# Performance work log

Hardware: AMD Instinct MI355X
Metric: run time of the kernel (lower is better)

The kernel has to match this reference:

```python
import jax, jax.numpy as jnp
import numpy as np

B, T, D, H = 2, 2048, 1024, 16
DK = D // H  # 64, head dim (even, required by RoPE pairing)


def setup_inputs() -> dict:
    key = jax.random.key(0)
    ks = jax.random.split(key, 9)
    sc = 1.0 / np.sqrt(D)
    x = jax.random.normal(ks[0], (B, T, D), jnp.float32)
    wq = jax.random.normal(ks[1], (D, D), jnp.float32) * sc
    bq = jax.random.normal(ks[2], (D,), jnp.float32) * 0.01
    wk = jax.random.normal(ks[3], (D, D), jnp.float32) * sc
    bk = jax.random.normal(ks[4], (D,), jnp.float32) * 0.01
    wv = jax.random.normal(ks[5], (D, D), jnp.float32) * sc
    bv = jax.random.normal(ks[6], (D,), jnp.float32) * 0.01
    wo = jax.random.normal(ks[7], (D, D), jnp.float32) * sc
    bo = jax.random.normal(ks[8], (D,), jnp.float32) * 0.01
    # causal mask, True = masked (matches masked_fill semantics); dim==3 -> broadcast over heads
    attn_mask = jnp.triu(jnp.ones((T, T), dtype=bool), 1)[None]  # [1,T,T]
    return dict(x=x, wq=wq, bq=bq, wk=wk, bk=bk, wv=wv, bv=bv, wo=wo, bo=bo,
                attn_mask=attn_mask)


def _rope(xh, sin, cos):
    # xh: [B,H,T,DK]; sin/cos: [T,DK/2]
    x1 = xh[..., 0::2]
    x2 = xh[..., 1::2]
    return jnp.stack([x1 * cos - x2 * sin, x1 * sin + x2 * cos], axis=-1).reshape(xh.shape)


def reference(x, wq, bq, wk, bk, wv, bv, wo, bo, attn_mask):
    q = (x @ wq.T + bq).reshape(B, T, H, DK).transpose(0, 2, 1, 3)  # [B,H,T,DK]
    k = (x @ wk.T + bk).reshape(B, T, H, DK).transpose(0, 2, 1, 3)
    v = (x @ wv.T + bv).reshape(B, T, H, DK).transpose(0, 2, 1, 3)
    # RoPE (seq_offset = 0)
    theta = 10000.0 ** (jnp.arange(0, DK, 2, dtype=jnp.float32) / DK)  # [DK/2]
    pos = jnp.arange(T, dtype=jnp.float32)[:, None]                    # [T,1]
    ang = pos / theta                                                  # [T,DK/2]
    sin, cos = jnp.sin(ang), jnp.cos(ang)
    q = _rope(q, sin, cos)
    k = _rope(k, sin, cos)
    # fp32 stable attention (inputs already fp32)
    scores = jnp.einsum('bhtd,bhsd->bhts', q, k) / np.sqrt(DK)
    scores = jnp.where(attn_mask[:, None], -1e9, scores)  # mask broadcast over heads
    attn = jax.nn.softmax(scores, axis=-1)
    ctx = jnp.einsum('bhts,bhsd->bhtd', attn, v)
    ctx = ctx.transpose(0, 2, 1, 3).reshape(B, T, D)
    return ctx @ wo.T + bo
```

## Files before the change

kernel.cpp:

```cpp
#include <hip/hip_runtime.h>
#include <stdint.h>
#include <stddef.h>

#define T_ 2048
#define D_ 1024
#define H_ 16

typedef __attribute__((ext_vector_type(8))) short short8;
typedef __attribute__((ext_vector_type(4))) float f32x4;
typedef __attribute__((ext_vector_type(4))) short s16x4;

__device__ __forceinline__ unsigned short f2bf(float f){
  union { float f; unsigned u; } c; c.f = f;
  unsigned u = c.u;
  return (unsigned short)((u + 0x7fffu + ((u >> 16) & 1u)) >> 16);
}

__device__ __forceinline__ unsigned pk_bf16(float lo, float hi){
  unsigned r;
  asm("v_cvt_pk_bf16_f32 %0, %1, %2" : "=v"(r) : "v"(lo), "v"(hi));
  return r;
}

__device__ __forceinline__ float fexp2(float x){
#if __has_builtin(__builtin_amdgcn_exp2f)
  return __builtin_amdgcn_exp2f(x);
#else
  return exp2f(x);
#endif
}

__device__ __forceinline__ f32x4 mfma16(short8 a, short8 b, f32x4 c){
  return __builtin_amdgcn_mfma_f32_16x16x32_bf16(a, b, c, 0, 0, 0);
}

__device__ __forceinline__ void gload16(const void* g, void* l){
  __builtin_amdgcn_global_load_lds(
      (const __attribute__((address_space(1))) unsigned*)g,
      (__attribute__((address_space(3))) unsigned*)l, 16, 0, 0);
}

__global__ __launch_bounds__(256) void k_prep(const float* __restrict__ x,
    const float* __restrict__ wq, const float* __restrict__ wk,
    const float* __restrict__ wv, const float* __restrict__ wo,
    unsigned short* __restrict__ xb, unsigned short* __restrict__ wqkv,
    unsigned short* __restrict__ wob, float* __restrict__ tab)
{
  if (blockIdx.x < 256){
    int i = blockIdx.x * 256 + threadIdx.x;
    int t = i >> 5, p = i & 31;
    float ang = (float)t * powf(10000.0f, -(float)p * (1.0f / 32.0f));
    tab[i] = sinf(ang);
    tab[T_ * 32 + i] = cosf(ang);
  }
  const long long NX = 4194304LL, NW = 1048576LL;
  long long base = ((long long)blockIdx.x * 256 + threadIdx.x) * 8;
  const float* s; unsigned short* d;
  if (base < NX){ s = x + base; d = xb + base; }
  else if (base < NX + 3*NW){
    long long j = base - NX;
    if (j < NW) s = wq + j;
    else if (j < 2*NW) s = wk + (j - NW);
    else s = wv + (j - 2*NW);
    d = wqkv + j;
  } else if (base < NX + 4*NW){
    long long j = base - NX - 3*NW;
    s = wo + j; d = wob + j;
  } else return;
  float4 a = *(const float4*)s;
  float4 b = *(const float4*)(s + 4);
  union { unsigned u[4]; short8 v; } o;
  o.u[0] = pk_bf16(a.x, a.y);
  o.u[1] = pk_bf16(a.z, a.w);
  o.u[2] = pk_bf16(b.x, b.y);
  o.u[3] = pk_bf16(b.z, b.w);
  *(short8*)d = o.v;
}

__device__ __forceinline__ void gemm_core(const unsigned short* __restrict__ A,
    const unsigned short* __restrict__ Bm, int m0, int n0,
    unsigned short* lA, unsigned short* lB, f32x4 (&acc)[4][4])
{
  const int tid = threadIdx.x, lane = tid & 63, wave = tid >> 6;
  const int wr = wave >> 1, wc = wave & 1;
  for (int mi = 0; mi < 4; ++mi)
    for (int ni = 0; ni < 4; ++ni)
      acc[mi][ni] = (f32x4){0.f, 0.f, 0.f, 0.f};
  for (int k0 = 0; k0 < 1024; k0 += 64){
    __syncthreads();
#pragma unroll
    for (int p = 0; p < 4; ++p){
      int c = p * 256 + tid, r = c >> 3, s = c & 7;
      int gs = (s ^ (r & 7)) << 3;
      gload16(A + (size_t)(m0 + r) * 1024 + k0 + gs, lA + c * 8);
      gload16(Bm + (size_t)(n0 + r) * 1024 + k0 + gs, lB + c * 8);
    }
    __syncthreads();
#pragma unroll
    for (int kk = 0; kk < 2; ++kk){
      int kslot = kk * 4 + (lane >> 4);
      short8 af[4], bf[4];
#pragma unroll
      for (int mi = 0; mi < 4; ++mi){
        int row = wr * 64 + mi * 16 + (lane & 15);
        af[mi] = *(const short8*)(lA + row * 64 + ((kslot ^ (row & 7)) << 3));
      }
#pragma unroll
      for (int ni = 0; ni < 4; ++ni){
        int row = wc * 64 + ni * 16 + (lane & 15);
        bf[ni] = *(const short8*)(lB + row * 64 + ((kslot ^ (row & 7)) << 3));
      }
#pragma unroll
      for (int mi = 0; mi < 4; ++mi)
#pragma unroll
        for (int ni = 0; ni < 4; ++ni)
          acc[mi][ni] = mfma16(af[mi], bf[ni], acc[mi][ni]);
    }
  }
}

__global__ __launch_bounds__(256) void k_qkv(const unsigned short* __restrict__ xb,
    const unsigned short* __restrict__ wqkv,
    const float* __restrict__ bq, const float* __restrict__ bk, const float* __restrict__ bv,
    const float* __restrict__ tab,
    unsigned short* __restrict__ Qw, unsigned short* __restrict__ Kw,
    unsigned short* __restrict__ Vw)
{
  __shared__ alignas(16) unsigned short lA[128 * 64];
  __shared__ alignas(16) unsigned short lB[128 * 64];
  int m0 = blockIdx.y * 128, n0 = blockIdx.x * 128;
  f32x4 acc[4][4];
  gemm_core(xb, wqkv, m0, n0, lA, lB, acc);
  int lane = threadIdx.x & 63, wave = threadIdx.x >> 6;
  int wr = wave >> 1, wc = wave & 1;
  int mat = n0 >> 10;
  const float* bias = (mat == 0) ? bq : (mat == 1 ? bk : bv);
  const float* st = tab; const float* ct = tab + T_ * 32;
  if (mat < 2){
    unsigned short* Out = (mat == 0) ? Qw : Kw;
    float qs = (mat == 0) ? 0.18033688011116f : 1.0f;
    for (int mi = 0; mi < 4; ++mi){
      for (int ni = 0; ni < 4; ++ni){
        int col = n0 + wc * 64 + ni * 16 + (lane & 15);
        int nn = col & 1023, h = nn >> 6, dd = nn & 63;
        float bsv = bias[nn];
        f32x4 v4 = acc[mi][ni];
#pragma unroll
        for (int r = 0; r < 4; ++r){
          int m = m0 + wr * 64 + mi * 16 + ((lane >> 4) << 2) + r;
          int bb = m >> 11, t = m & 2047;
          float v = v4[r] + bsv;
          float u = __shfl_xor(v, 1);
          int p = dd >> 1;
          float sv = st[t * 32 + p], cv = ct[t * 32 + p];
          float res = (dd & 1) ? (u * sv + v * cv) : (v * cv - u * sv);
          Out[((size_t)(bb * H_ + h) * T_ + t) * 64 + dd] = f2bf(res * qs);
        }
      }
    }
  } else {
    for (int mi = 0; mi < 4; ++mi){
      for (int ni = 0; ni < 4; ++ni){
        int col = n0 + wc * 64 + ni * 16 + (lane & 15);
        int nn = col & 1023, h = nn >> 6, dd = nn & 63;
        float bsv = bias[nn];
        int mb = m0 + wr * 64 + mi * 16 + ((lane >> 4) << 2);
        int bb = mb >> 11, t = mb & 2047;
        f32x4 v4 = acc[mi][ni];
        s16x4 o;
#pragma unroll
        for (int r = 0; r < 4; ++r) o[r] = (short)f2bf(v4[r] + bsv);
        *(s16x4*)(Vw + ((size_t)((bb * H_ + h) * 64 + dd)) * T_ + t) = o;
      }
    }
  }
}

__global__ __launch_bounds__(256) void k_attn(const unsigned short* __restrict__ Qw,
    const unsigned short* __restrict__ Kw, const unsigned short* __restrict__ Vt_g,
    unsigned short* __restrict__ ctxb)
{
  __shared__ alignas(16) unsigned short Kl0[128 * 64];
  __shared__ alignas(16) unsigned short Vl0[64 * 128];
  __shared__ alignas(16) unsigned short Kl1[128 * 64];
  __shared__ alignas(16) unsigned short Vl1[64 * 128];
  int qt = (int)gridDim.y - 1 - (int)blockIdx.y;
  int bh = blockIdx.x;
  int tid = threadIdx.x, lane = tid & 63, wave = tid >> 6;
  const unsigned short* Qb = Qw + (size_t)bh * T_ * 64;
  const unsigned short* Kb = Kw + (size_t)bh * T_ * 64;
  const unsigned short* Vb = Vt_g + (size_t)bh * 64 * T_;
  int q0 = qt * 128 + wave * 32;

  short8 qf[2][2];
#pragma unroll
  for (int mi = 0; mi < 2; ++mi){
    const unsigned short* qp = Qb + (size_t)(q0 + mi * 16 + (lane & 15)) * 64 + ((lane >> 4) << 3);
    qf[mi][0] = *(const short8*)qp;
    qf[mi][1] = *(const short8*)(qp + 32);
  }
  float mr[2] = {-1e30f, -1e30f}, lr[2] = {0.f, 0.f};
  f32x4 acc_o[2][4];
#pragma unroll
  for (int mi = 0; mi < 2; ++mi)
#pragma unroll
    for (int df = 0; df < 4; ++df) acc_o[mi][df] = (f32x4){0.f, 0.f, 0.f, 0.f};

  const int src0 = ((lane >> 4) & 1) * 32 + (lane & 15);
  const int src1 = src0 + 16;
  const bool hiHalf = lane >= 32;

  auto STAGE = [&](int j0, unsigned short* Kd, unsigned short* Vd){
#pragma unroll
    for (int p = 0; p < 4; ++p){
      int c = p * 256 + tid, r = c >> 3, s = c & 7;
      gload16(Kb + (size_t)(j0 + r) * 64 + ((s ^ (r & 7)) << 3), Kd + c * 8);
    }
#pragma unroll
    for (int p = 0; p < 4; ++p){
      int c = p * 256 + tid, r = c >> 4, s = c & 15;
      gload16(Vb + (size_t)r * T_ + j0 + ((s ^ (r & 7)) << 3), Vd + c * 8);
    }
  };

  auto COMPUTE = [&](int j0, const unsigned short* Kc, const unsigned short* Vc){
    bool need_mask = (j0 + 127 > q0);
    f32x4 accs[2][8];
#pragma unroll
    for (int mi = 0; mi < 2; ++mi)
#pragma unroll
      for (int jf = 0; jf < 8; ++jf) accs[mi][jf] = (f32x4){0.f, 0.f, 0.f, 0.f};
#pragma unroll
    for (int kk = 0; kk < 2; ++kk){
      int kslot = kk * 4 + (lane >> 4);
      short8 kf[8];
#pragma unroll
      for (int jf = 0; jf < 8; ++jf){
        int row = jf * 16 + (lane & 15);
        kf[jf] = *(const short8*)(Kc + row * 64 + ((kslot ^ (row & 7)) << 3));
      }
#pragma unroll
      for (int mi = 0; mi < 2; ++mi)
#pragma unroll
        for (int jf = 0; jf < 8; ++jf)
          accs[mi][jf] = mfma16(kf[jf], qf[mi][kk], accs[mi][jf]);
    }

    unsigned w0[2][8], w1[2][8];
#pragma unroll
    for (int mi = 0; mi < 2; ++mi){
      int qa = q0 + mi * 16 + (lane & 15);
      float mx = -1e30f;
#pragma unroll
      for (int jf = 0; jf < 8; ++jf)
#pragma unroll
        for (int r = 0; r < 4; ++r){
          float sv = accs[mi][jf][r];
          if (need_mask){
            int ja = j0 + jf * 16 + ((lane >> 4) << 2) + r;
            if (ja > qa) sv = -1e30f;
          }
          accs[mi][jf][r] = sv;
          mx = fmaxf(mx, sv);
        }
      mx = fmaxf(mx, __shfl_xor(mx, 16));
      mx = fmaxf(mx, __shfl_xor(mx, 32));
      float mn = fmaxf(mr[mi], mx);
      float sc = fexp2(mr[mi] - mn);
      mr[mi] = mn;
      float rs = 0.f;
#pragma unroll
      for (int jf = 0; jf < 8; ++jf)
#pragma unroll
        for (int r = 0; r < 4; ++r){
          float pe = fexp2(accs[mi][jf][r] - mn);
          accs[mi][jf][r] = pe;
          rs += pe;
        }
      rs += __shfl_xor(rs, 16);
      rs += __shfl_xor(rs, 32);
      lr[mi] = lr[mi] * sc + rs;
#pragma unroll
      for (int df = 0; df < 4; ++df){
        f32x4 a = acc_o[mi][df];
        a[0] *= sc; a[1] *= sc; a[2] *= sc; a[3] *= sc;
        acc_o[mi][df] = a;
      }
#pragma unroll
      for (int jf = 0; jf < 8; ++jf){
        w0[mi][jf] = pk_bf16(accs[mi][jf][0], accs[mi][jf][1]);
        w1[mi][jf] = pk_bf16(accs[mi][jf][2], accs[mi][jf][3]);
      }
    }

#pragma unroll
    for (int kk = 0; kk < 4; ++kk){
      int jslot = kk * 4 + (lane >> 4);
      short8 vf[4];
#pragma unroll
      for (int df = 0; df < 4; ++df){
        int row = df * 16 + (lane & 15);
        vf[df] = *(const short8*)(Vc + row * 128 + ((jslot ^ (row & 7)) << 3));
      }
#pragma unroll
      for (int mi = 0; mi < 2; ++mi){
        unsigned lo0 = (unsigned)__shfl((int)w0[mi][2*kk],   src0);
        unsigned hi0 = (unsigned)__shfl((int)w0[mi][2*kk+1], src0);
        unsigned lo1 = (unsigned)__shfl((int)w1[mi][2*kk],   src0);
        unsigned hi1 = (unsigned)__shfl((int)w1[mi][2*kk+1], src0);
        unsigned lo2 = (unsigned)__shfl((int)w0[mi][2*kk],   src1);
        unsigned hi2 = (unsigned)__shfl((int)w0[mi][2*kk+1], src1);
        unsigned lo3 = (unsigned)__shfl((int)w1[mi][2*kk],   src1);
        unsigned hi3 = (unsigned)__shfl((int)w1[mi][2*kk+1], src1);
        union { unsigned u[4]; short8 v; } pb;
        pb.u[0] = hiHalf ? hi0 : lo0;
        pb.u[1] = hiHalf ? hi1 : lo1;
        pb.u[2] = hiHalf ? hi2 : lo2;
        pb.u[3] = hiHalf ? hi3 : lo3;
#pragma unroll
        for (int df = 0; df < 4; ++df)
          acc_o[mi][df] = mfma16(vf[df], pb.v, acc_o[mi][df]);
      }
    }
  };

  int ntiles = qt + 1;
  STAGE(0, Kl0, Vl0);
  asm volatile("s_waitcnt vmcnt(0)" ::: "memory");
  __builtin_amdgcn_s_barrier();
  for (int jt = 0; jt < ntiles; ++jt){
    bool ev = !(jt & 1);
    unsigned short* Kc = ev ? Kl0 : Kl1;
    unsigned short* Vc = ev ? Vl0 : Vl1;
    if (jt + 1 < ntiles)
      STAGE((jt + 1) * 128, ev ? Kl1 : Kl0, ev ? Vl1 : Vl0);
    if (jt * 128 <= q0 + 31)
      COMPUTE(jt * 128, Kc, Vc);
    asm volatile("s_waitcnt vmcnt(0)" ::: "memory");
    __builtin_amdgcn_s_barrier();
  }

  int bb = bh >> 4, h = bh & 15;
#pragma unroll
  for (int mi = 0; mi < 2; ++mi){
    float inv = 1.0f / lr[mi];
    int t = q0 + mi * 16 + (lane & 15);
#pragma unroll
    for (int df = 0; df < 4; ++df){
      int d0 = df * 16 + ((lane >> 4) << 2);
      f32x4 a = acc_o[mi][df];
      s16x4 o;
#pragma unroll
      for (int r = 0; r < 4; ++r) o[r] = (short)f2bf(a[r] * inv);
      *(s16x4*)(ctxb + ((size_t)(bb * T_ + t)) * 1024 + h * 64 + d0) = o;
    }
  }
}

__global__ __launch_bounds__(256) void k_oproj(const unsigned short* __restrict__ ctxb,
    const unsigned short* __restrict__ wob, const float* __restrict__ bo,
    float* __restrict__ out)
{
  __shared__ alignas(16) unsigned short lA[128 * 64];
  __shared__ alignas(16) unsigned short lB[128 * 64];
  int m0 = blockIdx.y * 128, n0 = blockIdx.x * 128;
  f32x4 acc[4][4];
  gemm_core(ctxb, wob, m0, n0, lA, lB, acc);
  int lane = threadIdx.x & 63, wave = threadIdx.x >> 6;
  int wr = wave >> 1, wc = wave & 1;
  for (int mi = 0; mi < 4; ++mi)
    for (int ni = 0; ni < 4; ++ni){
      int col = n0 + wc * 64 + ni * 16 + (lane & 15);
      float bsv = bo[col];
      f32x4 v4 = acc[mi][ni];
#pragma unroll
      for (int r = 0; r < 4; ++r){
        int m = m0 + wr * 64 + mi * 16 + ((lane >> 4) << 2) + r;
        out[(size_t)m * 1024 + col] = v4[r] + bsv;
      }
    }
}

extern "C" void kernel_launch(void* const* d_in, const int* in_sizes, int n_in,
                              void* d_out, int out_size, void* d_ws, size_t ws_size,
                              hipStream_t stream)
{
  const float* x  = (const float*)d_in[0];
  const float* wq = (const float*)d_in[1];
  const float* bq = (const float*)d_in[2];
  const float* wk = (const float*)d_in[3];
  const float* bk = (const float*)d_in[4];
  const float* wv = (const float*)d_in[5];
  const float* bv = (const float*)d_in[6];
  const float* wo = (const float*)d_in[7];
  const float* bo = (const float*)d_in[8];
  char* w = (char*)d_ws;
  unsigned short* xb   = (unsigned short*)(w);
  unsigned short* wqkv = (unsigned short*)(w + (8 << 20));
  unsigned short* wob  = (unsigned short*)(w + (14 << 20));
  unsigned short* Qw   = (unsigned short*)(w + (16 << 20));
  unsigned short* Kw   = (unsigned short*)(w + (24 << 20));
  unsigned short* Vw   = (unsigned short*)(w + (32 << 20));
  unsigned short* ctxb = (unsigned short*)(w + (40 << 20));
  float* tab           = (float*)(w + (48 << 20));

  k_prep<<<4096, 256, 0, stream>>>(x, wq, wk, wv, wo, xb, wqkv, wob, tab);
  k_qkv<<<dim3(24, 32), 256, 0, stream>>>(xb, wqkv, bq, bk, bv, tab, Qw, Kw, Vw);
  k_attn<<<dim3(32, 16), 256, 0, stream>>>(Qw, Kw, Vw, ctxb);
  k_oproj<<<dim3(8, 32), 256, 0, stream>>>(ctxb, wob, bo, (float*)d_out);
}
```

Measured before the change: 136.4 us.

## Double-buffer LDS tiles in GEMM core to overlap global loads with MFMA

The shared GEMM core used by the QKV and output projections now ping-pongs between two LDS buffers. It issues the direct-to-LDS loads for the next K tile before computing on the current one, and uses a single waitcnt plus barrier per iteration instead of two syncthreads. The goal is to hide global memory latency behind MFMA work. In exchange, LDS use per block doubles to 64KB, which may lower occupancy.

After: 130.0 us. -4.7%, faster.

```diff
diff --git a/kernel.cpp b/kernel.cpp
--- a/kernel.cpp
+++ b/kernel.cpp
@@ -79,15 +79,16 @@
 
 __device__ __forceinline__ void gemm_core(const unsigned short* __restrict__ A,
     const unsigned short* __restrict__ Bm, int m0, int n0,
-    unsigned short* lA, unsigned short* lB, f32x4 (&acc)[4][4])
+    unsigned short* lA0, unsigned short* lB0,
+    unsigned short* lA1, unsigned short* lB1, f32x4 (&acc)[4][4])
 {
   const int tid = threadIdx.x, lane = tid & 63, wave = tid >> 6;
   const int wr = wave >> 1, wc = wave & 1;
   for (int mi = 0; mi < 4; ++mi)
     for (int ni = 0; ni < 4; ++ni)
       acc[mi][ni] = (f32x4){0.f, 0.f, 0.f, 0.f};
-  for (int k0 = 0; k0 < 1024; k0 += 64){
-    __syncthreads();
+
+  auto STAGE = [&](int k0, unsigned short* lA, unsigned short* lB){
 #pragma unroll
     for (int p = 0; p < 4; ++p){
       int c = p * 256 + tid, r = c >> 3, s = c & 7;
@@ -95,7 +96,8 @@
       gload16(A + (size_t)(m0 + r) * 1024 + k0 + gs, lA + c * 8);
       gload16(Bm + (size_t)(n0 + r) * 1024 + k0 + gs, lB + c * 8);
     }
-    __syncthreads();
+  };
+  auto COMPUTE = [&](const unsigned short* lA, const unsigned short* lB){
 #pragma unroll
     for (int kk = 0; kk < 2; ++kk){
       int kslot = kk * 4 + (lane >> 4);
@@ -116,6 +118,18 @@
         for (int ni = 0; ni < 4; ++ni)
           acc[mi][ni] = mfma16(af[mi], bf[ni], acc[mi][ni]);
     }
+  };
+
+  STAGE(0, lA0, lB0);
+  asm volatile("s_waitcnt vmcnt(0)" ::: "memory");
+  __builtin_amdgcn_s_barrier();
+  for (int k0 = 0; k0 < 1024; k0 += 64){
+    bool ev = !((k0 >> 6) & 1);
+    if (k0 + 64 < 1024)
+      STAGE(k0 + 64, ev ? lA1 : lA0, ev ? lB1 : lB0);
+    COMPUTE(ev ? lA0 : lA1, ev ? lB0 : lB1);
+    asm volatile("s_waitcnt vmcnt(0)" ::: "memory");
+    __builtin_amdgcn_s_barrier();
   }
 }
 
@@ -126,11 +140,13 @@
     unsigned short* __restrict__ Qw, unsigned short* __restrict__ Kw,
     unsigned short* __restrict__ Vw)
 {
-  __shared__ alignas(16) unsigned short lA[128 * 64];
-  __shared__ alignas(16) unsigned short lB[128 * 64];
+  __shared__ alignas(16) unsigned short lA0[128 * 64];
+  __shared__ alignas(16) unsigned short lB0[128 * 64];
+  __shared__ alignas(16) unsigned short lA1[128 * 64];
+  __shared__ alignas(16) unsigned short lB1[128 * 64];
   int m0 = blockIdx.y * 128, n0 = blockIdx.x * 128;
   f32x4 acc[4][4];
-  gemm_core(xb, wqkv, m0, n0, lA, lB, acc);
+  gemm_core(xb, wqkv, m0, n0, lA0, lB0, lA1, lB1, acc);
   int lane = threadIdx.x & 63, wave = threadIdx.x >> 6;
   int wr = wave >> 1, wc = wave & 1;
   int mat = n0 >> 10;
@@ -361,11 +377,13 @@
     const unsigned short* __restrict__ wob, const float* __restrict__ bo,
     float* __restrict__ out)
 {
-  __shared__ alignas(16) unsigned short lA[128 * 64];
-  __shared__ alignas(16) unsigned short lB[128 * 64];
+  __shared__ alignas(16) unsigned short lA0[128 * 64];
+  __shared__ alignas(16) unsigned short lB0[128 * 64];
+  __shared__ alignas(16) unsigned short lA1[128 * 64];
+  __shared__ alignas(16) unsigned short lB1[128 * 64];
   int m0 = blockIdx.y * 128, n0 = blockIdx.x * 128;
   f32x4 acc[4][4];
-  gemm_core(ctxb, wob, m0, n0, lA, lB, acc);
+  gemm_core(ctxb, wob, m0, n0, lA0, lB0, lA1, lB1, acc);
   int lane = threadIdx.x & 63, wave = threadIdx.x >> 6;
   int wr = wave >> 1, wc = wave & 1;
   for (int mi = 0; mi < 4; ++mi)
```
